# Kernel optimization log

Hardware: AMD Instinct MI355X
Metric: run time of the kernel (lower is better)

## Reference

```python
import jax, jax.numpy as jnp
import numpy as np

NEG_INF = -1e30

def _rotary_tables(n_pos, d_k):
    # angular_freq = (1/10000)**linspace(0,1,d_k//4), padded with d_k//4 zeros -> d_k//2 freqs
    freqs = (1.0 / 10000.0) ** jnp.linspace(0.0, 1.0, d_k // 4, dtype=jnp.float32)
    freqs = jnp.concatenate([freqs, jnp.zeros(d_k // 4, dtype=jnp.float32)])  # [d_k//2]
    t = jnp.arange(n_pos, dtype=jnp.float32)
    theta = t[:, None] * freqs[None, :]  # [n_pos, d_k//2]
    return jnp.cos(theta), jnp.sin(theta)

def _apply_rotary(x_bhtd, cos, sin):
    # Faithful to torch source: cos/sin are indexed/broadcast along dim -3,
    # which for [B,H,T,D] input is the HEAD axis (original code's quirk).
    c = cos[None, :, None, :]  # [1,H,1,D/2]
    s = sin[None, :, None, :]
    x1, x2 = jnp.split(x_bhtd, 2, axis=-1)
    y1 = x1 * c + x2 * s
    y2 = -x1 * s + x2 * c
    return jnp.concatenate([y1, y2], axis=-1)

def setup_inputs() -> dict:
    key = jax.random.key(0)
    k1, k2, k3 = jax.random.split(key, 3)
    B, S, D = 4, 2048, 2048
    x = jax.random.normal(k1, (B, S, D), dtype=jnp.float32)
    Wqkv = jax.random.normal(k2, (D, 3 * D), dtype=jnp.float32) * (D ** -0.5)
    Wo = jax.random.normal(k3, (D, D), dtype=jnp.float32) * (D ** -0.5)
    return {"x": x, "Wqkv": Wqkv, "Wo": Wo, "n_heads": 16}

def reference(x, Wqkv, Wo, n_heads):
    B, S, D = x.shape
    H = int(n_heads)
    d_k = D // H
    qkv = (x @ Wqkv).reshape(B, S, 3, H, d_k)
    qkv = jnp.transpose(qkv, (2, 0, 3, 1, 4))  # [3,B,H,S,dk]
    Q, K, V = qkv[0], qkv[1], qkv[2]
    cos, sin = _rotary_tables(H, d_k)  # indexed by head axis, per original code
    Q = _apply_rotary(Q, cos, sin)
    K = _apply_rotary(K, cos, sin)
    scores = jnp.einsum('bhqd,bhkd->bhqk', Q, K) / jnp.sqrt(jnp.float32(d_k))
    causal = jnp.tril(jnp.ones((S, S), dtype=bool))
    scores = jnp.where(causal[None, None, :, :], scores, NEG_INF)
    attn = jax.nn.softmax(scores, axis=-1)
    out = jnp.einsum('bhqk,bhkd->bhqd', attn, V)  # [B,H,S,dk]
    out = jnp.transpose(out, (0, 2, 1, 3)).reshape(B, S, D)
    return out @ Wo
```

## Files before the change

### kernel.cpp

```cpp
#include <hip/hip_runtime.h>

typedef __attribute__((ext_vector_type(8))) short short8;
typedef __attribute__((ext_vector_type(4))) short short4v;
typedef __attribute__((ext_vector_type(4))) float f32x4;

__device__ inline short f2bf(float f) {
    union { float f; unsigned u; } v; v.f = f;
    unsigned r = v.u + 0x7fffu + ((v.u >> 16) & 1u);
    return (short)(r >> 16);
}

__device__ __forceinline__ void gload16(const short* g, short* l) {
    __builtin_amdgcn_global_load_lds(
        (const __attribute__((address_space(1))) unsigned int*)g,
        (__attribute__((address_space(3))) unsigned int*)l, 16, 0, 0);
}

__global__ __launch_bounds__(256) void cvt_f32_to_bf16(const float* __restrict__ in,
                                                       short* __restrict__ out, int n4) {
    int i = blockIdx.x * 256 + threadIdx.x;
    if (i >= n4) return;
    float4 v = ((const float4*)in)[i];
    short4v o;
    o[0] = f2bf(v.x); o[1] = f2bf(v.y); o[2] = f2bf(v.z); o[3] = f2bf(v.w);
    ((short4v*)out)[i] = o;
}

__global__ __launch_bounds__(256) void transpose_to_bf16(const float* __restrict__ in,
                                                         short* __restrict__ out,
                                                         int R, int C) {
    __shared__ short tile[64][66];
    int r0 = blockIdx.x * 64, c0 = blockIdx.y * 64;
    int tid = threadIdx.x;
#pragma unroll
    for (int i = 0; i < 16; i++) {
        int idx = i * 256 + tid;
        int r = idx >> 6, c = idx & 63;
        tile[r][c] = f2bf(in[(size_t)(r0 + r) * C + (c0 + c)]);
    }
    __syncthreads();
#pragma unroll
    for (int i = 0; i < 16; i++) {
        int idx = i * 256 + tid;
        int c = idx >> 6, r = idx & 63;
        out[(size_t)(c0 + c) * R + (r0 + r)] = tile[r][c];
    }
}

template <int EPI>
__global__ __launch_bounds__(256) void gemm_bt(const short* __restrict__ A,
                                               const short* __restrict__ Bt,
                                               int M, int N, int K,
                                               short* __restrict__ O0, short* __restrict__ O1,
                                               short* __restrict__ O2, float* __restrict__ OF,
                                               float qscale) {
    __shared__ short Als[128 * 64];
    __shared__ short Bls[128 * 64];
    int tid = threadIdx.x;
    int lane = tid & 63, wid = tid >> 6;
    int wr = wid >> 1, wc = wid & 1;
    int ntn = N >> 7;
    int mt = blockIdx.x / ntn, nt = blockIdx.x % ntn;
    int row0 = mt << 7, col0 = nt << 7;
    int t15 = lane & 15, t4 = lane >> 4;
    int lrow = lane >> 3;
    int schunk = (lane & 7) ^ lrow;

    f32x4 acc[4][4];
#pragma unroll
    for (int m = 0; m < 4; m++)
#pragma unroll
        for (int n = 0; n < 4; n++) acc[m][n] = (f32x4){0.f, 0.f, 0.f, 0.f};

    for (int k0 = 0; k0 < K; k0 += 64) {
        __syncthreads();
#pragma unroll
        for (int i = 0; i < 4; i++) {
            int seg = wid * 4 + i;
            int row = seg * 8 + lrow;
            gload16(A + (size_t)(row0 + row) * K + k0 + schunk * 8, Als + seg * 512);
            gload16(Bt + (size_t)(col0 + row) * K + k0 + schunk * 8, Bls + seg * 512);
        }
        __syncthreads();
#pragma unroll
        for (int ks = 0; ks < 2; ks++) {
            short8 af[4], bfr[4];
#pragma unroll
            for (int m = 0; m < 4; m++) {
                int row = wr * 64 + m * 16 + t15;
                int ck = (ks * 4 + t4) ^ (row & 7);
                af[m] = *(short8*)(Als + row * 64 + ck * 8);
            }
#pragma unroll
            for (int n = 0; n < 4; n++) {
                int row = wc * 64 + n * 16 + t15;
                int ck = (ks * 4 + t4) ^ (row & 7);
                bfr[n] = *(short8*)(Bls + row * 64 + ck * 8);
            }
#pragma unroll
            for (int m = 0; m < 4; m++)
#pragma unroll
                for (int n = 0; n < 4; n++)
                    acc[m][n] = __builtin_amdgcn_mfma_f32_16x16x32_bf16(af[m], bfr[n], acc[m][n], 0, 0, 0);
        }
    }

#pragma unroll
    for (int m = 0; m < 4; m++) {
#pragma unroll
        for (int n = 0; n < 4; n++) {
#pragma unroll
            for (int r = 0; r < 4; r++) {
                float v = acc[m][n][r];
                int gm = row0 + wr * 64 + m * 16 + t4 * 4 + r;
                int gn = col0 + wc * 64 + n * 16 + t15;
                if (EPI == 0) {
                    int part = gn >> 11, within = gn & 2047;
                    int h = within >> 7, dk = within & 127;
                    int b = gm >> 11, s = gm & 2047;
                    int z = b * 16 + h;
                    if (part == 0) O0[((size_t)z * 2048 + s) * 128 + dk] = f2bf(v * qscale);
                    else if (part == 1) O1[((size_t)z * 2048 + s) * 128 + dk] = f2bf(v);
                    else O2[((size_t)z * 128 + dk) * 2048 + s] = f2bf(v);
                } else {
                    OF[(size_t)gm * N + gn] = v;
                }
            }
        }
    }
}

__global__ __launch_bounds__(512, 4) void attn_fwd(const short* __restrict__ Q,
                                                   const short* __restrict__ Kb,
                                                   const short* __restrict__ Vt,
                                                   short* __restrict__ O) {
    __shared__ short Kls[2][64 * 128];
    __shared__ short Vls[128 * 64];
    __shared__ short Pls[8][16 * 72];
    int tid = threadIdx.x, lane = tid & 63, wid = tid >> 6;
    int bx = blockIdx.x, z = blockIdx.y;
    int pr = bx >> 1, hh = bx & 1;
    int qpan = (wid < 4) ? pr : (15 - pr);
    int t15 = lane & 15, t4 = lane >> 4;
    const short* Qh = Q + (size_t)z * 2048 * 128;
    const short* Kh = Kb + (size_t)z * 2048 * 128;
    const short* Vh = Vt + (size_t)z * 128 * 2048;
    int q0w = qpan * 128 + hh * 64 + (wid & 3) * 16;

    short8 qf[4];
    {
        const short* qrow = Qh + (size_t)(q0w + t15) * 128;
#pragma unroll
        for (int s = 0; s < 4; s++) qf[s] = *(const short8*)(qrow + s * 32 + t4 * 8);
    }

    f32x4 o[8];
#pragma unroll
    for (int st = 0; st < 8; st++) o[st] = (f32x4){0.f, 0.f, 0.f, 0.f};
    float m_r[4], l_r[4];
#pragma unroll
    for (int r = 0; r < 4; r++) { m_r[r] = -1e30f; l_r[r] = 0.f; }

    auto stageK = [&](int t, int buf) {
#pragma unroll
        for (int i = 0; i < 2; i++) {
            int seg = wid * 2 + i;
            int row = seg * 4 + t4;
            int kl = (lane & 15) ^ (row & 7);
            gload16(Kh + (size_t)(t * 64 + row) * 128 + kl * 8, &Kls[buf][seg * 512]);
        }
    };
    auto stageV = [&](int t) {
#pragma unroll
        for (int i = 0; i < 2; i++) {
            int seg = wid * 2 + i;
            int row = seg * 8 + (lane >> 3);
            int kl = (lane & 7) ^ (row & 7);
            gload16(Vh + (size_t)row * 2048 + t * 64 + kl * 8, &Vls[seg * 512]);
        }
    };

    int nt = 2 * (15 - pr) + 2;
    stageK(0, 0);
    __syncthreads();

    for (int t = 0; t < nt; t++) {
        int buf = t & 1;
        stageV(t);
        bool active = (t * 64 <= q0w + 15);

        if (active) {
            f32x4 sc[4];
#pragma unroll
            for (int c = 0; c < 4; c++) {
                sc[c] = (f32x4){0.f, 0.f, 0.f, 0.f};
#pragma unroll
                for (int s = 0; s < 4; s++) {
                    int row = c * 16 + t15;
                    int ck = (s * 4 + t4) ^ (row & 7);
                    short8 kf = *(short8*)(&Kls[buf][row * 128 + ck * 8]);
                    sc[c] = __builtin_amdgcn_mfma_f32_16x16x32_bf16(qf[s], kf, sc[c], 0, 0, 0);
                }
            }

            if (t * 64 + 63 > q0w) {
#pragma unroll
                for (int c = 0; c < 4; c++)
#pragma unroll
                    for (int r = 0; r < 4; r++) {
                        int kv = t * 64 + c * 16 + t15, qq = q0w + t4 * 4 + r;
                        if (kv > qq) sc[c][r] = -1e30f;
                    }
            }

            float tm[4];
#pragma unroll
            for (int r = 0; r < 4; r++)
                tm[r] = fmaxf(fmaxf(sc[0][r], sc[1][r]), fmaxf(sc[2][r], sc[3][r]));
            bool need = (tm[0] > m_r[0] + 8.f) | (tm[1] > m_r[1] + 8.f) |
                        (tm[2] > m_r[2] + 8.f) | (tm[3] > m_r[3] + 8.f);
            if (__any(need)) {
#pragma unroll
                for (int r = 0; r < 4; r++) {
#pragma unroll
                    for (int msk = 1; msk <= 8; msk <<= 1)
                        tm[r] = fmaxf(tm[r], __shfl_xor(tm[r], msk));
                    float mn = fmaxf(m_r[r], tm[r]);
                    float scf = __expf(m_r[r] - mn);
                    m_r[r] = mn;
                    l_r[r] *= scf;
#pragma unroll
                    for (int st = 0; st < 8; st++) o[st][r] *= scf;
                }
            }
#pragma unroll
            for (int r = 0; r < 4; r++) {
#pragma unroll
                for (int c = 0; c < 4; c++) {
                    float pv = __expf(sc[c][r] - m_r[r]);
                    Pls[wid][(t4 * 4 + r) * 72 + c * 16 + t15] = f2bf(pv);
                    l_r[r] += pv;
                }
            }
        }

        __syncthreads();
        if (t + 1 < nt) stageK(t + 1, buf ^ 1);

        if (active) {
            short8 pa[2];
#pragma unroll
            for (int s2 = 0; s2 < 2; s2++)
                pa[s2] = *(short8*)(&Pls[wid][0] + t15 * 72 + s2 * 32 + t4 * 8);
#pragma unroll
            for (int st = 0; st < 8; st++) {
#pragma unroll
                for (int s2 = 0; s2 < 2; s2++) {
                    int row = st * 16 + t15;
                    int ck = (s2 * 4 + t4) ^ (row & 7);
                    short8 vf = *(short8*)(&Vls[row * 64 + ck * 8]);
                    o[st] = __builtin_amdgcn_mfma_f32_16x16x32_bf16(pa[s2], vf, o[st], 0, 0, 0);
                }
            }
        }

        __syncthreads();
    }

#pragma unroll
    for (int r = 0; r < 4; r++)
#pragma unroll
        for (int msk = 1; msk <= 8; msk <<= 1)
            l_r[r] += __shfl_xor(l_r[r], msk);

    int b = z >> 4, h = z & 15;
#pragma unroll
    for (int st = 0; st < 8; st++)
#pragma unroll
        for (int r = 0; r < 4; r++) {
            int s = q0w + t4 * 4 + r;
            float val = o[st][r] / l_r[r];
            O[((size_t)b * 2048 + s) * 2048 + h * 128 + st * 16 + t15] = f2bf(val);
        }
}

extern "C" void kernel_launch(void* const* d_in, const int* in_sizes, int n_in,
                              void* d_out, int out_size, void* d_ws, size_t ws_size,
                              hipStream_t stream) {
    const float* x = (const float*)d_in[0];
    const float* Wqkv = (const float*)d_in[1];
    const float* Wo = (const float*)d_in[2];

    const int B = 4, S = 2048, D = 2048, DK = 128;
    const int M = B * S;
    const int N1 = 3 * D;
    (void)in_sizes; (void)n_in; (void)out_size; (void)ws_size;

    char* ws = (char*)d_ws;
    size_t off = 0;
    short* x_bf = (short*)(ws + off);   off += (size_t)M * D * 2;
    short* wqkv_t = (short*)(ws + off); off += (size_t)N1 * D * 2;
    short* wo_t = (short*)(ws + off);   off += (size_t)D * D * 2;
    short* Qb = (short*)(ws + off);     off += (size_t)64 * S * DK * 2;
    short* Kb = (short*)(ws + off);     off += (size_t)64 * S * DK * 2;
    short* Vt = (short*)(ws + off);     off += (size_t)64 * S * DK * 2;
    short* Ob = (short*)(ws + off);     off += (size_t)M * D * 2;

    cvt_f32_to_bf16<<<(M * D / 4 + 255) / 256, 256, 0, stream>>>(x, x_bf, M * D / 4);
    transpose_to_bf16<<<dim3(D / 64, N1 / 64, 1), 256, 0, stream>>>(Wqkv, wqkv_t, D, N1);
    transpose_to_bf16<<<dim3(D / 64, D / 64, 1), 256, 0, stream>>>(Wo, wo_t, D, D);
    gemm_bt<0><<<(M / 128) * (N1 / 128), 256, 0, stream>>>(
        x_bf, wqkv_t, M, N1, D, Qb, Kb, Vt, nullptr, 0.08838834764831845f);
    attn_fwd<<<dim3(16, 64), 512, 0, stream>>>(Qb, Kb, Vt, Ob);
    gemm_bt<1><<<(M / 128) * (D / 128), 256, 0, stream>>>(
        Ob, wo_t, M, D, D, nullptr, nullptr, nullptr, (float*)d_out, 1.0f);
}
```

Before: 515.9 us.

## Rewrite GEMM with 256x256 tiles, triple-buffered LDS pipeline and XCD-aware block remap

The GEMM kernel moves from a 128x128 tile with 256 threads and a single LDS buffer to a 256x256 tile with 512 threads. It also uses a three-stage ring of LDS buffers filled asynchronously under explicit vmcnt waits, and remaps block IDs so that neighbouring tiles land on the same XCD. The K step shrinks to 32 and the XOR swizzle is dropped. The goal is to overlap global loads with MFMA work and raise reuse per tile. The trade-offs are more register pressure from 128 accumulators, possible LDS bank conflicts without the swizzle, and fewer blocks, which hurts wave balance on the 2048-wide output projection.

```diff
diff --git a/kernel.cpp b/kernel.cpp
--- a/kernel.cpp
+++ b/kernel.cpp
@@ -48,77 +48,96 @@
 }
 
 template <int EPI>
-__global__ __launch_bounds__(256) void gemm_bt(const short* __restrict__ A,
-                                               const short* __restrict__ Bt,
-                                               int M, int N, int K,
-                                               short* __restrict__ O0, short* __restrict__ O1,
-                                               short* __restrict__ O2, float* __restrict__ OF,
-                                               float qscale) {
-    __shared__ short Als[128 * 64];
-    __shared__ short Bls[128 * 64];
+__global__ __launch_bounds__(512, 2) void gemm_bt(const short* __restrict__ A,
+                                                  const short* __restrict__ Bt,
+                                                  int M, int N, int K,
+                                                  short* __restrict__ O0, short* __restrict__ O1,
+                                                  short* __restrict__ O2, float* __restrict__ OF,
+                                                  float qscale) {
+    __shared__ short Als[3][256 * 32];
+    __shared__ short Bls[3][256 * 32];
     int tid = threadIdx.x;
     int lane = tid & 63, wid = tid >> 6;
-    int wr = wid >> 1, wc = wid & 1;
-    int ntn = N >> 7;
-    int mt = blockIdx.x / ntn, nt = blockIdx.x % ntn;
-    int row0 = mt << 7, col0 = nt << 7;
+    int wr = wid >> 2, wc = wid & 3;
+    int ntn = N >> 8;
+    int nwg = gridDim.x;
+    int cpx = nwg >> 3;
+    int bid = blockIdx.x;
+    int wgid = (bid & 7) * cpx + (bid >> 3);
+    int mt = wgid / ntn, nt = wgid % ntn;
+    int row0 = mt << 8, col0 = nt << 8;
     int t15 = lane & 15, t4 = lane >> 4;
-    int lrow = lane >> 3;
-    int schunk = (lane & 7) ^ lrow;
-
-    f32x4 acc[4][4];
-#pragma unroll
-    for (int m = 0; m < 4; m++)
+    int srow = lane >> 2, schunk = lane & 3;
+
+    f32x4 acc[8][4];
+#pragma unroll
+    for (int m = 0; m < 8; m++)
 #pragma unroll
         for (int n = 0; n < 4; n++) acc[m][n] = (f32x4){0.f, 0.f, 0.f, 0.f};
 
-    for (int k0 = 0; k0 < K; k0 += 64) {
-        __syncthreads();
-#pragma unroll
-        for (int i = 0; i < 4; i++) {
-            int seg = wid * 4 + i;
-            int row = seg * 8 + lrow;
-            gload16(A + (size_t)(row0 + row) * K + k0 + schunk * 8, Als + seg * 512);
-            gload16(Bt + (size_t)(col0 + row) * K + k0 + schunk * 8, Bls + seg * 512);
-        }
-        __syncthreads();
-#pragma unroll
-        for (int ks = 0; ks < 2; ks++) {
-            short8 af[4], bfr[4];
-#pragma unroll
-            for (int m = 0; m < 4; m++) {
-                int row = wr * 64 + m * 16 + t15;
-                int ck = (ks * 4 + t4) ^ (row & 7);
-                af[m] = *(short8*)(Als + row * 64 + ck * 8);
-            }
-#pragma unroll
-            for (int n = 0; n < 4; n++) {
-                int row = wc * 64 + n * 16 + t15;
-                int ck = (ks * 4 + t4) ^ (row & 7);
-                bfr[n] = *(short8*)(Bls + row * 64 + ck * 8);
-            }
-#pragma unroll
-            for (int m = 0; m < 4; m++)
-#pragma unroll
-                for (int n = 0; n < 4; n++)
-                    acc[m][n] = __builtin_amdgcn_mfma_f32_16x16x32_bf16(af[m], bfr[n], acc[m][n], 0, 0, 0);
-        }
-    }
-
-#pragma unroll
-    for (int m = 0; m < 4; m++) {
+    int NT = K >> 5;
+
+    auto stage = [&](int t, int b) {
+        int k0 = t << 5;
+#pragma unroll
+        for (int i = 0; i < 2; i++) {
+            int seg = wid * 2 + i;
+            int row = seg * 16 + srow;
+            gload16(A + (size_t)(row0 + row) * K + k0 + schunk * 8, &Als[b][seg * 512]);
+            gload16(Bt + (size_t)(col0 + row) * K + k0 + schunk * 8, &Bls[b][seg * 512]);
+        }
+    };
+
+    stage(0, 0);
+    stage(1, 1);
+
+    for (int t = 0; t < NT; t++) {
+        int b = t % 3;
+        if (t + 2 < NT) {
+            stage(t + 2, (t + 2) % 3);
+            asm volatile("s_waitcnt vmcnt(8)" ::: "memory");
+        } else if (t + 1 < NT) {
+            asm volatile("s_waitcnt vmcnt(4)" ::: "memory");
+        } else {
+            asm volatile("s_waitcnt vmcnt(0)" ::: "memory");
+        }
+        __builtin_amdgcn_s_barrier();
+        __builtin_amdgcn_sched_barrier(0);
+
+        short8 af[8], bfr[4];
+#pragma unroll
+        for (int m = 0; m < 8; m++)
+            af[m] = *(short8*)(&Als[b][(wr * 128 + m * 16 + t15) * 32 + t4 * 8]);
+#pragma unroll
+        for (int n = 0; n < 4; n++)
+            bfr[n] = *(short8*)(&Bls[b][(wc * 64 + n * 16 + t15) * 32 + t4 * 8]);
+
+        __builtin_amdgcn_s_setprio(1);
+#pragma unroll
+        for (int m = 0; m < 8; m++)
+#pragma unroll
+            for (int n = 0; n < 4; n++)
+                acc[m][n] = __builtin_amdgcn_mfma_f32_16x16x32_bf16(af[m], bfr[n], acc[m][n], 0, 0, 0);
+        __builtin_amdgcn_s_setprio(0);
+
+        __builtin_amdgcn_s_barrier();
+        __builtin_amdgcn_sched_barrier(0);
+    }
+
+#pragma unroll
+    for (int m = 0; m < 8; m++) {
 #pragma unroll
         for (int n = 0; n < 4; n++) {
 #pragma unroll
             for (int r = 0; r < 4; r++) {
                 float v = acc[m][n][r];
-                int gm = row0 + wr * 64 + m * 16 + t4 * 4 + r;
+                int gm = row0 + wr * 128 + m * 16 + t4 * 4 + r;
                 int gn = col0 + wc * 64 + n * 16 + t15;
                 if (EPI == 0) {
                     int part = gn >> 11, within = gn & 2047;
                     int h = within >> 7, dk = within & 127;
-                    int b = gm >> 11, s = gm & 2047;
-                    int z = b * 16 + h;
+                    int bb = gm >> 11, s = gm & 2047;
+                    int z = bb * 16 + h;
                     if (part == 0) O0[((size_t)z * 2048 + s) * 128 + dk] = f2bf(v * qscale);
                     else if (part == 1) O1[((size_t)z * 2048 + s) * 128 + dk] = f2bf(v);
                     else O2[((size_t)z * 128 + dk) * 2048 + s] = f2bf(v);
@@ -309,9 +328,9 @@
     cvt_f32_to_bf16<<<(M * D / 4 + 255) / 256, 256, 0, stream>>>(x, x_bf, M * D / 4);
     transpose_to_bf16<<<dim3(D / 64, N1 / 64, 1), 256, 0, stream>>>(Wqkv, wqkv_t, D, N1);
     transpose_to_bf16<<<dim3(D / 64, D / 64, 1), 256, 0, stream>>>(Wo, wo_t, D, D);
-    gemm_bt<0><<<(M / 128) * (N1 / 128), 256, 0, stream>>>(
+    gemm_bt<0><<<(M / 256) * (N1 / 256), 512, 0, stream>>>(
         x_bf, wqkv_t, M, N1, D, Qb, Kb, Vt, nullptr, 0.08838834764831845f);
     attn_fwd<<<dim3(16, 64), 512, 0, stream>>>(Qb, Kb, Vt, Ob);
-    gemm_bt<1><<<(M / 128) * (D / 128), 256, 0, stream>>>(
+    gemm_bt<1><<<(M / 256) * (D / 256), 512, 0, stream>>>(
         Ob, wo_t, M, D, D, nullptr, nullptr, nullptr, (float*)d_out, 1.0f);
 }
```

Result: slower. 545.1 us (+5.6%).

## Double-buffer GEMM LDS tiles and remap workgroups across XCDs

Applied to the files above, without the earlier changes.

The GEMM kernel now keeps two LDS buffers for the A and B tiles and prefetches the next K tile with global_load_lds while MFMAs run on the current one, with a single barrier per iteration instead of two. It also remaps block IDs so that consecutive tiles land on the same XCD, which is meant to improve L2 reuse. LDS use doubles to 64KB per block, which may lower occupancy. The remap assumes the grid size is divisible by 8.

```diff
diff --git a/kernel.cpp b/kernel.cpp
--- a/kernel.cpp
+++ b/kernel.cpp
@@ -54,13 +54,17 @@
                                                short* __restrict__ O0, short* __restrict__ O1,
                                                short* __restrict__ O2, float* __restrict__ OF,
                                                float qscale) {
-    __shared__ short Als[128 * 64];
-    __shared__ short Bls[128 * 64];
+    __shared__ short Als[2][128 * 64];
+    __shared__ short Bls[2][128 * 64];
     int tid = threadIdx.x;
     int lane = tid & 63, wid = tid >> 6;
     int wr = wid >> 1, wc = wid & 1;
     int ntn = N >> 7;
-    int mt = blockIdx.x / ntn, nt = blockIdx.x % ntn;
+    int nwg = gridDim.x;
+    int cpx = nwg >> 3;
+    int bid = blockIdx.x;
+    int wgid = (bid & 7) * cpx + (bid >> 3);
+    int mt = wgid / ntn, nt = wgid % ntn;
     int row0 = mt << 7, col0 = nt << 7;
     int t15 = lane & 15, t4 = lane >> 4;
     int lrow = lane >> 3;
@@ -72,16 +76,26 @@
 #pragma unroll
         for (int n = 0; n < 4; n++) acc[m][n] = (f32x4){0.f, 0.f, 0.f, 0.f};
 
-    for (int k0 = 0; k0 < K; k0 += 64) {
-        __syncthreads();
+    int NT = K >> 6;
+
+    auto stage = [&](int t, int b) {
+        int k0 = t << 6;
 #pragma unroll
         for (int i = 0; i < 4; i++) {
             int seg = wid * 4 + i;
             int row = seg * 8 + lrow;
-            gload16(A + (size_t)(row0 + row) * K + k0 + schunk * 8, Als + seg * 512);
-            gload16(Bt + (size_t)(col0 + row) * K + k0 + schunk * 8, Bls + seg * 512);
-        }
-        __syncthreads();
+            gload16(A + (size_t)(row0 + row) * K + k0 + schunk * 8, &Als[b][seg * 512]);
+            gload16(Bt + (size_t)(col0 + row) * K + k0 + schunk * 8, &Bls[b][seg * 512]);
+        }
+    };
+
+    stage(0, 0);
+    __syncthreads();
+
+    for (int t = 0; t < NT; t++) {
+        int b = t & 1;
+        if (t + 1 < NT) stage(t + 1, b ^ 1);
+
 #pragma unroll
         for (int ks = 0; ks < 2; ks++) {
             short8 af[4], bfr[4];
@@ -89,13 +103,13 @@
             for (int m = 0; m < 4; m++) {
                 int row = wr * 64 + m * 16 + t15;
                 int ck = (ks * 4 + t4) ^ (row & 7);
-                af[m] = *(short8*)(Als + row * 64 + ck * 8);
+                af[m] = *(short8*)(&Als[b][row * 64 + ck * 8]);
             }
 #pragma unroll
             for (int n = 0; n < 4; n++) {
                 int row = wc * 64 + n * 16 + t15;
                 int ck = (ks * 4 + t4) ^ (row & 7);
-                bfr[n] = *(short8*)(Bls + row * 64 + ck * 8);
+                bfr[n] = *(short8*)(&Bls[b][row * 64 + ck * 8]);
             }
 #pragma unroll
             for (int m = 0; m < 4; m++)
@@ -103,6 +117,8 @@
                 for (int n = 0; n < 4; n++)
                     acc[m][n] = __builtin_amdgcn_mfma_f32_16x16x32_bf16(af[m], bfr[n], acc[m][n], 0, 0, 0);
         }
+
+        __syncthreads();
     }
 
 #pragma unroll
@@ -117,8 +133,8 @@
                 if (EPI == 0) {
                     int part = gn >> 11, within = gn & 2047;
                     int h = within >> 7, dk = within & 127;
-                    int b = gm >> 11, s = gm & 2047;
-                    int z = b * 16 + h;
+                    int bb = gm >> 11, s = gm & 2047;
+                    int z = bb * 16 + h;
                     if (part == 0) O0[((size_t)z * 2048 + s) * 128 + dk] = f2bf(v * qscale);
                     else if (part == 1) O1[((size_t)z * 2048 + s) * 128 + dk] = f2bf(v);
                     else O2[((size_t)z * 128 + dk) * 2048 + s] = f2bf(v);
```

New measurement: 518.8 us. About the same (+0.6%).
